# Performance work log

Hardware: AMD Instinct MI355X
Metric: run time of the kernel (lower is better)

Reference implementation:

```python
import jax, jax.numpy as jnp
import numpy as np

DIM = 256
NUM_HEADS = 4
HEAD_DIM = DIM // NUM_HEADS  # 64
SCALE = HEAD_DIM ** -0.5


def _dwconv(x, w, b):
    # x: [B,H,W,C], w: [3,3,1,C] depthwise, stride 2, padding 1
    c = x.shape[-1]
    y = jax.lax.conv_general_dilated(
        x, w, window_strides=(2, 2), padding=((1, 1), (1, 1)),
        dimension_numbers=('NHWC', 'HWIO', 'NHWC'), feature_group_count=c)
    return y + b


def setup_inputs() -> dict:
    key = jax.random.key(0)
    ks = jax.random.split(key, 12)
    s = 0.02
    return {
        'x': jax.random.normal(ks[0], (8, 64, 64, DIM), jnp.float32),
        'q_w': jax.random.normal(ks[1], (DIM, DIM), jnp.float32) * s,
        'q_b': jnp.zeros((DIM,), jnp.float32),
        'k_w': jax.random.normal(ks[2], (DIM, HEAD_DIM), jnp.float32) * s,
        'k_b': jnp.zeros((HEAD_DIM,), jnp.float32),
        'v_w': jax.random.normal(ks[3], (DIM, HEAD_DIM), jnp.float32) * s,
        'v_b': jnp.zeros((HEAD_DIM,), jnp.float32),
        'kconv_w': jax.random.normal(ks[4], (3, 3, 1, HEAD_DIM), jnp.float32) * s,
        'kconv_b': jnp.zeros((HEAD_DIM,), jnp.float32),
        'vconv_w': jax.random.normal(ks[5], (3, 3, 1, HEAD_DIM), jnp.float32) * s,
        'vconv_b': jnp.zeros((HEAD_DIM,), jnp.float32),
        'out_w': jax.random.normal(ks[6], (DIM, DIM), jnp.float32) * s,
        'out_b': jnp.zeros((DIM,), jnp.float32),
    }


def reference(x, q_w, q_b, k_w, k_b, v_w, v_b,
              kconv_w, kconv_b, vconv_w, vconv_b, out_w, out_b):
    B, H, W, _ = x.shape
    S = H * W
    q = x @ q_w + q_b                      # [B,H,W,DIM]
    k = x @ k_w + k_b                      # [B,H,W,HEAD_DIM]
    v = x @ v_w + v_b
    k = _dwconv(k, kconv_w, kconv_b)       # [B,H/2,W/2,HEAD_DIM]
    v = _dwconv(v, vconv_w, vconv_b)
    Kv = (H // 2) * (W // 2)
    q = q.reshape(B, S, NUM_HEADS, HEAD_DIM)
    k = k.reshape(B, Kv, HEAD_DIM)
    v = v.reshape(B, Kv, HEAD_DIM)
    # MQA: single shared K/V head
    attn = jnp.einsum('bqhd,bkd->bhqk', q, k) * SCALE
    attn = jax.nn.softmax(attn, axis=-1)
    out = jnp.einsum('bhqk,bkd->bqhd', attn, v)   # [B,S,nh,hd]
    out = out.reshape(B, S, DIM) @ out_w + out_b
    return out.reshape(B, H, W, DIM)
```

## Files before the change

kernel.cpp:

```cpp
#include <hip/hip_runtime.h>
#include <hip/hip_bf16.h>

typedef __bf16 v8bf __attribute__((ext_vector_type(8)));
typedef float f32x4 __attribute__((ext_vector_type(4)));
typedef float f32x16 __attribute__((ext_vector_type(16)));
typedef int v2i __attribute__((ext_vector_type(2)));
typedef int v4i __attribute__((ext_vector_type(4)));

#define MFMA16(a, b, c) __builtin_amdgcn_mfma_f32_16x16x32_bf16(a, b, c, 0, 0, 0)
#define MFMA32(a, b, c) __builtin_amdgcn_mfma_f32_32x32x16_bf16(a, b, c, 0, 0, 0)
#define GLOAD16(gp, lp)                                                        \
  __builtin_amdgcn_global_load_lds(                                            \
      (const __attribute__((address_space(1))) void*)(gp),                     \
      (__attribute__((address_space(3))) void*)(lp), 16, 0, 0)

#define QSCALE 0.18033688011112042f

__global__ __launch_bounds__(256) void k_cvt_w(const float* __restrict__ qw,
                                               const float* __restrict__ kw,
                                               const float* __restrict__ vw,
                                               const float* __restrict__ ow,
                                               __bf16* __restrict__ wfrag,
                                               __bf16* __restrict__ owfrag) {
  int t = blockIdx.x * 256 + threadIdx.x;
  if (t < 98304) {
    int e = t & 7, idx = t >> 3;
    int l = idx & 63; idx >>= 6;
    int n = idx & 3; idx >>= 2;
    int kk = idx & 7, nb = idx >> 3;
    int nn = nb * 64 + n * 16 + (l & 15);
    int k = kk * 32 + 8 * (l >> 4) + e;
    float v;
    if (nn < 256) v = qw[k * 256 + nn] * QSCALE;
    else if (nn < 320) v = kw[k * 64 + (nn - 256)];
    else v = vw[k * 64 + (nn - 320)];
    wfrag[t] = (__bf16)v;
  } else {
    int u = t - 98304;
    int e = u & 7, idx = u >> 3;
    int l = idx & 63; idx >>= 6;
    int n = idx & 3; idx >>= 2;
    int kk = idx & 7, nb = idx >> 3;
    int nn = nb * 64 + n * 16 + (l & 15);
    int k = kk * 32 + 8 * (l >> 4) + e;
    owfrag[u] = (__bf16)ow[k * 256 + nn];
  }
}

__global__ __launch_bounds__(256) void k_qkv(const float* __restrict__ x,
                                             const __bf16* __restrict__ wfrag,
                                             const float* __restrict__ qb,
                                             const float* __restrict__ kb,
                                             const float* __restrict__ vb,
                                             __bf16* __restrict__ qo,
                                             __bf16* __restrict__ klin,
                                             __bf16* __restrict__ vlin) {
  int bx = blockIdx.x;
  int mb = (bx & 7) * 64 + (bx >> 3);
  int wave = threadIdx.x >> 6, lane = threadIdx.x & 63;
  int g = lane >> 4, c = lane & 15;
  int r0 = mb * 64 + wave * 16;
  const v8bf* wf = (const v8bf*)wfrag;

  v8bf a[8];
#pragma unroll
  for (int kk = 0; kk < 8; ++kk) {
    const float* ap = x + (size_t)(r0 + c) * 256 + kk * 32 + 8 * g;
    float4 f0 = *(const float4*)ap;
    float4 f1 = *(const float4*)(ap + 4);
    v8bf t;
    t[0] = (__bf16)f0.x; t[1] = (__bf16)f0.y; t[2] = (__bf16)f0.z; t[3] = (__bf16)f0.w;
    t[4] = (__bf16)f1.x; t[5] = (__bf16)f1.y; t[6] = (__bf16)f1.z; t[7] = (__bf16)f1.w;
    a[kk] = t;
  }
#pragma unroll
  for (int nb = 0; nb < 6; ++nb) {
    int n0 = nb * 64;
    f32x4 acc[4];
#pragma unroll
    for (int n = 0; n < 4; ++n) acc[n] = f32x4{0.f, 0.f, 0.f, 0.f};
#pragma unroll
    for (int kk = 0; kk < 8; ++kk) {
      v8bf bf[4];
#pragma unroll
      for (int n = 0; n < 4; ++n)
        bf[n] = wf[(((nb * 8 + kk) * 4 + n) << 6) | lane];
#pragma unroll
      for (int n = 0; n < 4; ++n) acc[n] = MFMA16(a[kk], bf[n], acc[n]);
    }
#pragma unroll
    for (int n = 0; n < 4; ++n) {
      int col = n0 + n * 16 + c;
      float bias;
      if (col < 256) bias = qb[col] * QSCALE;
      else if (col < 320) bias = kb[col - 256];
      else bias = vb[col - 320];
#pragma unroll
      for (int j = 0; j < 4; ++j) {
        int row = r0 + 4 * g + j;
        float v = acc[n][j] + bias;
        if (col < 256) qo[(size_t)row * 256 + col] = (__bf16)v;
        else if (col < 320) klin[(size_t)row * 64 + (col - 256)] = (__bf16)v;
        else vlin[(size_t)row * 64 + (col - 320)] = (__bf16)v;
      }
    }
  }
}

__global__ __launch_bounds__(256) void k_conv(const __bf16* __restrict__ klin,
                                              const __bf16* __restrict__ vlin,
                                              const float* __restrict__ kw,
                                              const float* __restrict__ kbias,
                                              const float* __restrict__ vw,
                                              const float* __restrict__ vbias,
                                              __bf16* __restrict__ kc,
                                              __bf16* __restrict__ vcT) {
  __shared__ __bf16 VT[32][66];
  int bx = blockIdx.x;
  int b = bx >> 5, pt = bx & 31;
  int t = threadIdx.x;
  int ch = t & 63, pg = t >> 6;
  float kwv[9], vwv[9];
#pragma unroll
  for (int i = 0; i < 9; ++i) { kwv[i] = kw[i * 64 + ch]; vwv[i] = vw[i * 64 + ch]; }
  float kb0 = kbias[ch], vb0 = vbias[ch];
  const __bf16* kin = klin + (size_t)b * 262144;
  const __bf16* vin = vlin + (size_t)b * 262144;
#pragma unroll
  for (int i = 0; i < 8; ++i) {
    int pl = pg * 8 + i;
    int p = pt * 32 + pl;
    int oy = p >> 5, ox = p & 31;
    float ak = kb0, av = vb0;
#pragma unroll
    for (int dy = 0; dy < 3; ++dy) {
      int iy = 2 * oy - 1 + dy;
      if (iy < 0 || iy > 63) continue;
#pragma unroll
      for (int dx = 0; dx < 3; ++dx) {
        int ix = 2 * ox - 1 + dx;
        if (ix < 0 || ix > 63) continue;
        size_t src = ((size_t)iy * 64 + ix) * 64 + ch;
        ak += (float)kin[src] * kwv[dy * 3 + dx];
        av += (float)vin[src] * vwv[dy * 3 + dx];
      }
    }
    kc[((size_t)b * 1024 + p) * 64 + ch] = (__bf16)ak;
    VT[pl][ch] = (__bf16)av;
  }
  __syncthreads();
  int row = t >> 2, c0 = (t & 3) * 8;
  __bf16 tmp[8];
#pragma unroll
  for (int i = 0; i < 8; ++i) tmp[i] = VT[c0 + i][row];
  *(v4i*)(vcT + (size_t)b * 65536 + row * 1024 + pt * 32 + c0) = *(v4i*)tmp;
}

__global__ __launch_bounds__(256) void k_repack(const __bf16* __restrict__ kc,
                                                const __bf16* __restrict__ vcT,
                                                __bf16* __restrict__ kcS,
                                                __bf16* __restrict__ vcS) {
  int b = blockIdx.x >> 5, tile = blockIdx.x & 31;
  int u = threadIdx.x;
  int kj = u >> 5, kr = (u & 31) ^ kj;
  v4i kv = *(const v4i*)(kc + (size_t)b * 65536 + (size_t)tile * 2048 +
                         kr * 64 + kj * 8);
  *(v4i*)(kcS + ((size_t)b * 32 + tile) * 2048 + u * 8) = kv;
  int dt = u >> 7, ks = (u >> 6) & 1, vh = (u >> 5) & 1;
  int cc = (u & 31) ^ (ks * 2 + vh);
  v4i vv = *(const v4i*)(vcT + (size_t)b * 65536 + (size_t)(dt * 32 + cc) * 1024 +
                         tile * 32 + ks * 16 + vh * 8);
  *(v4i*)(vcS + ((size_t)b * 32 + tile) * 2048 + u * 8) = vv;
}

__global__ __launch_bounds__(256) void k_attn(const __bf16* __restrict__ q,
                                              const __bf16* __restrict__ kcS,
                                              const __bf16* __restrict__ vcS,
                                              const __bf16* __restrict__ owfrag,
                                              const float* __restrict__ ob,
                                              float* __restrict__ out) {
  __shared__ __bf16 SMEM[12288];
  int bx = blockIdx.x;
  int L = (bx & 7) * 128 + (bx >> 3);
  int b = L >> 7, qt = L & 127;
  int wave = threadIdx.x >> 6, lane = threadIdx.x & 63;
  int c = lane & 31, hi = lane >> 5;
  int t = threadIdx.x;
  size_t rowBase = (size_t)b * 4096 + qt * 32;

  const __bf16* kg = kcS + (size_t)b * 65536 + t * 8;
  const __bf16* vg = vcS + (size_t)b * 65536 + t * 8;
  __bf16* kl = &SMEM[t * 8];
  __bf16* vl = &SMEM[2048 + t * 8];

  int Koff[4], Voff[2][2];
#pragma unroll
  for (int kk = 0; kk < 4; ++kk) {
    int j = kk * 2 + hi;
    Koff[kk] = (j * 32 + (c ^ j)) * 8;
  }
#pragma unroll
  for (int ks = 0; ks < 2; ++ks)
#pragma unroll
    for (int dt = 0; dt < 2; ++dt) {
      int j = ks * 2 + hi;
      Voff[ks][dt] = (256 + dt * 128 + ks * 64 + hi * 32 + (c ^ j)) * 8;
    }

  const __bf16* qbase = q + (rowBase + c) * 256 + wave * 64 + hi * 8;
  v8bf Qf[4];
#pragma unroll
  for (int kk = 0; kk < 4; ++kk) Qf[kk] = *(const v8bf*)(qbase + kk * 16);

  f32x16 O0 = {}, O1 = {};
  const f32x16 Z16 = {};
  float ls0 = 0.f, ls1 = 0.f, ls2 = 0.f, ls3 = 0.f;

  GLOAD16(kg, kl);
  GLOAD16(vg, vl);
  GLOAD16(kg + 2048, kl + 4096);
  GLOAD16(vg + 2048, vl + 4096);

  int cur = 0;
  int nxt2 = 2;
  for (int it = 0; it < 32; ++it) {
    if (it < 31) {
      asm volatile("s_waitcnt vmcnt(2)" ::: "memory");
    } else {
      asm volatile("s_waitcnt vmcnt(0)" ::: "memory");
    }
    __builtin_amdgcn_sched_barrier(0);
    __builtin_amdgcn_s_barrier();
    __builtin_amdgcn_sched_barrier(0);
    if (it < 30) {
      GLOAD16(kg + (it + 2) * 2048, kl + nxt2 * 4096);
      GLOAD16(vg + (it + 2) * 2048, vl + nxt2 * 4096);
    }

    const __bf16* base = &SMEM[cur * 4096];
    v8bf Kf[4], Vf[2][2];
#pragma unroll
    for (int kk = 0; kk < 4; ++kk) Kf[kk] = *(const v8bf*)(base + Koff[kk]);
#pragma unroll
    for (int ks = 0; ks < 2; ++ks)
#pragma unroll
      for (int dt = 0; dt < 2; ++dt)
        Vf[ks][dt] = *(const v8bf*)(base + Voff[ks][dt]);

    f32x16 S = MFMA32(Kf[0], Qf[0], Z16);
    S = MFMA32(Kf[1], Qf[1], S);
    S = MFMA32(Kf[2], Qf[2], S);
    S = MFMA32(Kf[3], Qf[3], S);

#pragma unroll
    for (int r = 0; r < 16; ++r) S[r] = __builtin_amdgcn_exp2f(S[r]);
    ls0 += (S[0] + S[1]) + (S[2] + S[3]);
    ls1 += (S[4] + S[5]) + (S[6] + S[7]);
    ls2 += (S[8] + S[9]) + (S[10] + S[11]);
    ls3 += (S[12] + S[13]) + (S[14] + S[15]);

    int w[8];
#pragma unroll
    for (int q2 = 0; q2 < 8; ++q2) {
      int r;
      asm("v_cvt_pk_bf16_f32 %0, %1, %2"
          : "=v"(r) : "v"(S[2 * q2]), "v"(S[2 * q2 + 1]));
      w[q2] = r;
    }
    v2i s1 = __builtin_amdgcn_permlane32_swap(w[2], w[0], false, false);
    v2i s2 = __builtin_amdgcn_permlane32_swap(w[3], w[1], false, false);
    v2i s3 = __builtin_amdgcn_permlane32_swap(w[6], w[4], false, false);
    v2i s4 = __builtin_amdgcn_permlane32_swap(w[7], w[5], false, false);
    v4i pa0i, pa1i;
    pa0i[0] = s1[1]; pa0i[1] = s2[1]; pa0i[2] = s1[0]; pa0i[3] = s2[0];
    pa1i[0] = s3[1]; pa1i[1] = s4[1]; pa1i[2] = s3[0]; pa1i[3] = s4[0];
    v8bf pa0 = *(v8bf*)&pa0i, pa1 = *(v8bf*)&pa1i;

    O0 = MFMA32(pa0, Vf[0][0], O0);
    O1 = MFMA32(pa0, Vf[0][1], O1);
    O0 = MFMA32(pa1, Vf[1][0], O0);
    O1 = MFMA32(pa1, Vf[1][1], O1);

    cur = (cur == 2) ? 0 : cur + 1;
    nxt2 = (nxt2 == 2) ? 0 : nxt2 + 1;
  }

  float lsum = (ls0 + ls1) + (ls2 + ls3);
  float tot = lsum + __shfl_xor(lsum, 32);
  float linv = 1.0f / tot;

  __syncthreads();

  __bf16(*Ot)[264] = (__bf16(*)[264])SMEM;
#pragma unroll
  for (int r = 0; r < 16; ++r) {
    int qr = (r & 3) + 8 * (r >> 2) + 4 * hi;
    float li = __shfl(linv, qr);
    Ot[qr][wave * 64 + c] = (__bf16)(O0[r] * li);
    Ot[qr][wave * 64 + 32 + c] = (__bf16)(O1[r] * li);
  }
  __syncthreads();

  int g = lane >> 4, c16 = lane & 15;
  const v8bf* wf = (const v8bf*)owfrag;
  f32x4 acc[2][4];
#pragma unroll
  for (int m = 0; m < 2; ++m)
#pragma unroll
    for (int n = 0; n < 4; ++n) acc[m][n] = f32x4{0.f, 0.f, 0.f, 0.f};
#pragma unroll
  for (int kk = 0; kk < 8; ++kk) {
    v8bf a0 = *(const v8bf*)&Ot[c16][kk * 32 + 8 * g];
    v8bf a1 = *(const v8bf*)&Ot[16 + c16][kk * 32 + 8 * g];
    v8bf bf[4];
#pragma unroll
    for (int n = 0; n < 4; ++n)
      bf[n] = wf[(((wave * 8 + kk) * 4 + n) << 6) | lane];
#pragma unroll
    for (int n = 0; n < 4; ++n) {
      acc[0][n] = MFMA16(a0, bf[n], acc[0][n]);
      acc[1][n] = MFMA16(a1, bf[n], acc[1][n]);
    }
  }
#pragma unroll
  for (int n = 0; n < 4; ++n) {
    int col = wave * 64 + n * 16 + c16;
    float bias = ob[col];
#pragma unroll
    for (int m = 0; m < 2; ++m)
#pragma unroll
      for (int j = 0; j < 4; ++j) {
        int row = m * 16 + 4 * g + j;
        out[(rowBase + row) * 256 + col] = acc[m][n][j] + bias;
      }
  }
}

extern "C" void kernel_launch(void* const* d_in, const int* in_sizes, int n_in,
                              void* d_out, int out_size, void* d_ws, size_t ws_size,
                              hipStream_t stream) {
  const float* x   = (const float*)d_in[0];
  const float* qw  = (const float*)d_in[1];
  const float* qb  = (const float*)d_in[2];
  const float* kw  = (const float*)d_in[3];
  const float* kb  = (const float*)d_in[4];
  const float* vw  = (const float*)d_in[5];
  const float* vb  = (const float*)d_in[6];
  const float* kcw = (const float*)d_in[7];
  const float* kcb = (const float*)d_in[8];
  const float* vcw = (const float*)d_in[9];
  const float* vcb = (const float*)d_in[10];
  const float* ow  = (const float*)d_in[11];
  const float* ob  = (const float*)d_in[12];
  float* out = (float*)d_out;
  char* ws = (char*)d_ws;

  __bf16* kcS    = (__bf16*)(ws + 0);
  __bf16* vcS    = (__bf16*)(ws + 1048576);
  __bf16* qbuf   = (__bf16*)(ws + 16777216);
  __bf16* klin   = (__bf16*)(ws + 33554432);
  __bf16* vlin   = (__bf16*)(ws + 37748736);
  __bf16* kc     = (__bf16*)(ws + 41943040);
  __bf16* vcT    = (__bf16*)(ws + 42991616);
  __bf16* wfrag  = (__bf16*)(ws + 44040192);
  __bf16* owfrag = (__bf16*)(ws + 44236800);

  k_cvt_w<<<640, 256, 0, stream>>>(qw, kw, vw, ow, wfrag, owfrag);
  k_qkv<<<512, 256, 0, stream>>>(x, wfrag, qb, kb, vb, qbuf, klin, vlin);
  k_conv<<<256, 256, 0, stream>>>(klin, vlin, kcw, kcb, vcw, vcb, kc, vcT);
  k_repack<<<256, 256, 0, stream>>>(kc, vcT, kcS, vcS);
  k_attn<<<1024, 256, 0, stream>>>(qbuf, kcS, vcS, owfrag, ob, out);
}
```

Baseline: 95.56 us.

## Fuse depthwise conv with K/V repack and raise MFMA wave priority

The depthwise conv kernel now writes K and V directly in the swizzled tile layouts the attention kernel consumes. This removes the separate repack kernel, the intermediate kc/vcT buffers and the shared-memory transpose. K is computed with 8-channel vector loads per thread, while V uses scalar per-channel loads with a strided access pattern. The attention loop also wraps its MFMA sequences in s_setprio to favour matrix-issuing waves, which may or may not help scheduling.

```diff
diff --git a/kernel.cpp b/kernel.cpp
--- a/kernel.cpp
+++ b/kernel.cpp
@@ -113,64 +113,67 @@
                                               const float* __restrict__ kbias,
                                               const float* __restrict__ vw,
                                               const float* __restrict__ vbias,
-                                              __bf16* __restrict__ kc,
-                                              __bf16* __restrict__ vcT) {
-  __shared__ __bf16 VT[32][66];
+                                              __bf16* __restrict__ kcS,
+                                              __bf16* __restrict__ vcS) {
   int bx = blockIdx.x;
-  int b = bx >> 5, pt = bx & 31;
-  int t = threadIdx.x;
-  int ch = t & 63, pg = t >> 6;
-  float kwv[9], vwv[9];
-#pragma unroll
-  for (int i = 0; i < 9; ++i) { kwv[i] = kw[i * 64 + ch]; vwv[i] = vw[i * 64 + ch]; }
-  float kb0 = kbias[ch], vb0 = vbias[ch];
+  int b = bx >> 5, tile = bx & 31;
+  int u = threadIdx.x;
   const __bf16* kin = klin + (size_t)b * 262144;
   const __bf16* vin = vlin + (size_t)b * 262144;
-#pragma unroll
-  for (int i = 0; i < 8; ++i) {
-    int pl = pg * 8 + i;
-    int p = pt * 32 + pl;
-    int oy = p >> 5, ox = p & 31;
-    float ak = kb0, av = vb0;
+
+  {
+    int kj = u >> 5, kr = (u & 31) ^ kj;
+    float acc[8];
+#pragma unroll
+    for (int e = 0; e < 8; ++e) acc[e] = kbias[kj * 8 + e];
 #pragma unroll
     for (int dy = 0; dy < 3; ++dy) {
-      int iy = 2 * oy - 1 + dy;
+      int iy = 2 * tile - 1 + dy;
       if (iy < 0 || iy > 63) continue;
 #pragma unroll
       for (int dx = 0; dx < 3; ++dx) {
-        int ix = 2 * ox - 1 + dx;
+        int ix = 2 * kr - 1 + dx;
         if (ix < 0 || ix > 63) continue;
-        size_t src = ((size_t)iy * 64 + ix) * 64 + ch;
-        ak += (float)kin[src] * kwv[dy * 3 + dx];
-        av += (float)vin[src] * vwv[dy * 3 + dx];
+        v8bf kv8 = *(const v8bf*)(kin + ((size_t)iy * 64 + ix) * 64 + kj * 8);
+        const float* wp = kw + (dy * 3 + dx) * 64 + kj * 8;
+#pragma unroll
+        for (int e = 0; e < 8; ++e) acc[e] += (float)kv8[e] * wp[e];
       }
     }
-    kc[((size_t)b * 1024 + p) * 64 + ch] = (__bf16)ak;
-    VT[pl][ch] = (__bf16)av;
-  }
-  __syncthreads();
-  int row = t >> 2, c0 = (t & 3) * 8;
-  __bf16 tmp[8];
-#pragma unroll
-  for (int i = 0; i < 8; ++i) tmp[i] = VT[c0 + i][row];
-  *(v4i*)(vcT + (size_t)b * 65536 + row * 1024 + pt * 32 + c0) = *(v4i*)tmp;
-}
-
-__global__ __launch_bounds__(256) void k_repack(const __bf16* __restrict__ kc,
-                                                const __bf16* __restrict__ vcT,
-                                                __bf16* __restrict__ kcS,
-                                                __bf16* __restrict__ vcS) {
-  int b = blockIdx.x >> 5, tile = blockIdx.x & 31;
-  int u = threadIdx.x;
-  int kj = u >> 5, kr = (u & 31) ^ kj;
-  v4i kv = *(const v4i*)(kc + (size_t)b * 65536 + (size_t)tile * 2048 +
-                         kr * 64 + kj * 8);
-  *(v4i*)(kcS + ((size_t)b * 32 + tile) * 2048 + u * 8) = kv;
-  int dt = u >> 7, ks = (u >> 6) & 1, vh = (u >> 5) & 1;
-  int cc = (u & 31) ^ (ks * 2 + vh);
-  v4i vv = *(const v4i*)(vcT + (size_t)b * 65536 + (size_t)(dt * 32 + cc) * 1024 +
-                         tile * 32 + ks * 16 + vh * 8);
-  *(v4i*)(vcS + ((size_t)b * 32 + tile) * 2048 + u * 8) = vv;
+    __bf16 o[8];
+#pragma unroll
+    for (int e = 0; e < 8; ++e) o[e] = (__bf16)acc[e];
+    *(v4i*)(kcS + ((size_t)b * 32 + tile) * 2048 + u * 8) = *(v4i*)o;
+  }
+
+  {
+    int dt = u >> 7, ks = (u >> 6) & 1, vh = (u >> 5) & 1;
+    int cc = (u & 31) ^ (ks * 2 + vh);
+    int ch = dt * 32 + cc;
+    float vwv[9];
+#pragma unroll
+    for (int i = 0; i < 9; ++i) vwv[i] = vw[i * 64 + ch];
+    float vb0 = vbias[ch];
+    __bf16 o[8];
+#pragma unroll
+    for (int e = 0; e < 8; ++e) {
+      int ox = ks * 16 + vh * 8 + e;
+      float av = vb0;
+#pragma unroll
+      for (int dy = 0; dy < 3; ++dy) {
+        int iy = 2 * tile - 1 + dy;
+        if (iy < 0 || iy > 63) continue;
+#pragma unroll
+        for (int dx = 0; dx < 3; ++dx) {
+          int ix = 2 * ox - 1 + dx;
+          if (ix < 0 || ix > 63) continue;
+          av += (float)vin[((size_t)iy * 64 + ix) * 64 + ch] * vwv[dy * 3 + dx];
+        }
+      }
+      o[e] = (__bf16)av;
+    }
+    *(v4i*)(vcS + ((size_t)b * 32 + tile) * 2048 + u * 8) = *(v4i*)o;
+  }
 }
 
 __global__ __launch_bounds__(256) void k_attn(const __bf16* __restrict__ q,
@@ -247,10 +250,12 @@
       for (int dt = 0; dt < 2; ++dt)
         Vf[ks][dt] = *(const v8bf*)(base + Voff[ks][dt]);
 
+    __builtin_amdgcn_s_setprio(1);
     f32x16 S = MFMA32(Kf[0], Qf[0], Z16);
     S = MFMA32(Kf[1], Qf[1], S);
     S = MFMA32(Kf[2], Qf[2], S);
     S = MFMA32(Kf[3], Qf[3], S);
+    __builtin_amdgcn_s_setprio(0);
 
 #pragma unroll
     for (int r = 0; r < 16; ++r) S[r] = __builtin_amdgcn_exp2f(S[r]);
@@ -276,10 +281,12 @@
     pa1i[0] = s3[1]; pa1i[1] = s4[1]; pa1i[2] = s3[0]; pa1i[3] = s4[0];
     v8bf pa0 = *(v8bf*)&pa0i, pa1 = *(v8bf*)&pa1i;
 
+    __builtin_amdgcn_s_setprio(1);
     O0 = MFMA32(pa0, Vf[0][0], O0);
     O1 = MFMA32(pa0, Vf[0][1], O1);
     O0 = MFMA32(pa1, Vf[1][0], O0);
     O1 = MFMA32(pa1, Vf[1][1], O1);
+    __builtin_amdgcn_s_setprio(0);
 
     cur = (cur == 2) ? 0 : cur + 1;
     nxt2 = (nxt2 == 2) ? 0 : nxt2 + 1;
@@ -360,14 +367,11 @@
   __bf16* qbuf   = (__bf16*)(ws + 16777216);
   __bf16* klin   = (__bf16*)(ws + 33554432);
   __bf16* vlin   = (__bf16*)(ws + 37748736);
-  __bf16* kc     = (__bf16*)(ws + 41943040);
-  __bf16* vcT    = (__bf16*)(ws + 42991616);
   __bf16* wfrag  = (__bf16*)(ws + 44040192);
   __bf16* owfrag = (__bf16*)(ws + 44236800);
 
   k_cvt_w<<<640, 256, 0, stream>>>(qw, kw, vw, ow, wfrag, owfrag);
   k_qkv<<<512, 256, 0, stream>>>(x, wfrag, qb, kb, vb, qbuf, klin, vlin);
-  k_conv<<<256, 256, 0, stream>>>(klin, vlin, kcw, kcb, vcw, vcb, kc, vcT);
-  k_repack<<<256, 256, 0, stream>>>(kc, vcT, kcS, vcS);
+  k_conv<<<256, 256, 0, stream>>>(klin, vlin, kcw, kcb, vcw, vcb, kcS, vcS);
   k_attn<<<1024, 256, 0, stream>>>(qbuf, kcS, vcS, owfrag, ob, out);
 }
```

Result: no change. 97.27 us (+1.8%).
